# Performance work log

Hardware: AMD Instinct MI355X
Metric: run time of the kernel (lower is better)

## Reference

```python
import jax, jax.numpy as jnp
import numpy as np

NLAT = 192  # octahedral O96-class grid


def _lons(nlat):
    half = [20 + 4 * i for i in range(nlat // 2)]
    return half + half[::-1]


def _dft_matrix(nlat, mmax):
    # Truncated per-ring real-DFT basis (torch.fft.rfft convention, 'forward' 1/n norm).
    # Ring j has nlon_j points; frequencies beyond its Nyquist (m > nlon_j//2) are zero.
    lons = _lons(nlat)
    max_nlon = max(lons)
    D = np.zeros((nlat, max_nlon, mmax), dtype=np.complex64)
    for j, n in enumerate(lons):
        keep = min(mmax, n // 2 + 1)
        k = np.arange(n)[:, None]
        m = np.arange(keep)[None, :]
        D[j, :n, :keep] = np.exp(-2j * np.pi * k * m / n) / n
    return D


def _legendre_weights(nlat, lmax, mmax):
    # Orthonormalized associated Legendre P_l^m at Gaussian latitudes (north->south),
    # with Gaussian quadrature weights and the 2*pi longitude factor folded in.
    xg, wg = np.polynomial.legendre.leggauss(nlat)
    x = xg[::-1].copy()
    w = wg[::-1].copy()
    s = np.sqrt(1.0 - x * x)
    leg = np.zeros((lmax, mmax, nlat))
    pmm = np.full(nlat, 1.0 / np.sqrt(4.0 * np.pi))
    for m in range(mmax):
        if m > 0:
            pmm = -np.sqrt((2 * m + 1) / (2.0 * m)) * s * pmm
        if m < lmax:
            leg[m, m] = pmm
        if m + 1 < lmax:
            leg[m + 1, m] = np.sqrt(2 * m + 3.0) * x * pmm
        for l in range(m + 2, lmax):
            a = np.sqrt((4.0 * l * l - 1.0) / (l * l - m * m))
            bb = np.sqrt(((2.0 * l + 1.0) * (l - 1 + m) * (l - 1 - m)) / ((2.0 * l - 3.0) * (l * l - m * m)))
            leg[l, m] = a * x * leg[l - 1, m] - bb * leg[l - 2, m]
    leg = 2.0 * np.pi * leg * w[None, None, :]
    return leg.astype(np.float32)


def setup_inputs() -> dict:
    key = jax.random.key(0)
    nlat = NLAT
    lmax = mmax = nlat // 2
    n_points = sum(_lons(nlat))  # 40320 for nlat=192
    data = jax.random.normal(key, (4, 1, 1, n_points, 100), dtype=jnp.float32)
    dft = jnp.asarray(_dft_matrix(nlat, mmax))
    leg = jnp.asarray(_legendre_weights(nlat, lmax, mmax))
    return {"data": data, "dft": dft, "leg": leg}


def reference(data, dft, leg):
    b, t, e, p, v = data.shape
    nlat, max_nlon, mmax = dft.shape
    lmax = leg.shape[0]
    lons = _lons(nlat)
    # static scatter map: flattened ragged rings -> [nlat, max_nlon] padded layout
    flat_idx = np.concatenate([j * max_nlon + np.arange(n) for j, n in enumerate(lons)])
    x = jnp.transpose(data, (0, 1, 2, 4, 3)).reshape(-1, p)  # [(b t e v), p]
    B = x.shape[0]
    x_pad = jnp.zeros((B, nlat * max_nlon), x.dtype).at[:, flat_idx].set(x)
    x_pad = x_pad.reshape(B, nlat, max_nlon)
    # ragged per-ring truncated real DFT, then associated-Legendre contraction
    f_hat = jnp.einsum('bjn,jnm->bjm', x_pad, dft)        # [B, nlat, mmax] complex
    coeffs = jnp.einsum('bjm,lmj->blm', f_hat, leg)       # [B, lmax, mmax] complex
    coeffs = coeffs.reshape(b, t, e, v, lmax, mmax)
    return jnp.transpose(coeffs, (0, 1, 2, 4, 5, 3))      # [b, t, e, yF, xF, v]
```

## Files before the change

### kernel.cpp

```cpp
#include <hip/hip_runtime.h>

#define NLAT 192
#define NPTS 40320
#define MMAX 96
#define LMAX 96
#define NV   100
#define MAXN 400
#define NB   400

typedef __attribute__((ext_vector_type(8))) short short8v;
typedef __attribute__((ext_vector_type(4))) float f32x4;

#define FSTR 40

static __device__ __forceinline__ float bits2f(unsigned int b) {
    union { unsigned int i; float f; } v; v.i = b; return v.f;
}
static __device__ __forceinline__ unsigned int f2bf(float f) {
    union { float f; unsigned int i; } v; v.f = f;
    return (v.i + 0x7FFFu + ((v.i >> 16) & 1u)) >> 16;
}

static __device__ __forceinline__ int Ssum(int n) {
    int q = n >> 3, r = n & 7; return 4 * q * (q - 1) + q * r;
}
static __device__ __forceinline__ int atoffk(int j) {
    if (j < 96) return 32 * (Ssum(j + 12) - 4);
    return 32 * (672 + 676 - Ssum(204 - j));
}
static __device__ __forceinline__ int kpad_of(int j) {
    return 32 * ((j < 96 ? (j + 12) : (203 - j)) >> 3);
}

typedef const __attribute__((address_space(1))) void* gas_ptr;
typedef __attribute__((address_space(3))) void* las_ptr;
static __device__ __forceinline__ void gload_lds16(const void* g, void* l) {
    __builtin_amdgcn_global_load_lds((gas_ptr)g, (las_ptr)l, 16, 0, 0);
}

__global__ __launch_bounds__(256) void leg_conv_kernel(
    const float* __restrict__ leg,
    unsigned short* __restrict__ legh,
    unsigned short* __restrict__ legl)
{
    int idx = blockIdx.x * 256 + threadIdx.x;
    if (idx >= 96 * 96 * 192) return;
    int j = idx % 192;
    int lm = idx / 192;
    int m = lm % 96, l = lm / 96;
    float v = leg[idx];
    unsigned int h = f2bf(v);
    unsigned int lo = f2bf(v - bits2f(h << 16));
    size_t o = ((size_t)m * 96 + l) * 192 + j;
    legh[o] = (unsigned short)h;
    legl[o] = (unsigned short)lo;
}

__global__ __launch_bounds__(256) void dft_transpose_kernel(
    const unsigned int* __restrict__ dftw,
    unsigned short* __restrict__ At)
{
    const int j = blockIdx.x;
    const int kpad = kpad_of(j);
    const int t = blockIdx.y;
    const int k0 = t * 32;
    if (k0 >= kpad) return;
    const int n = j < 96 ? 20 + 4 * j : 400 - 4 * (j - 96);
    unsigned short* abase = At + (size_t)atoffk(j) * 192 + (size_t)t * 6144;
    const int tid = threadIdx.x;
#pragma unroll
    for (int s = 0; s < 3; ++s) {
        int slot = s * 256 + tid;
        int row = slot % 192;
        int ch  = slot / 192;
        int m = row < 96 ? row : row - 96;
        bool isIm = row >= 96;
        const unsigned int* dp = dftw + ((size_t)j * MAXN + k0 + ch * 8) * 96 + m;
        unsigned short o[8];
#pragma unroll
        for (int i = 0; i < 8; ++i) {
            int k = k0 + ch * 8 + i;
            unsigned int v = (k < n) ? dp[(size_t)i * 96] : 0u;
            o[i] = isIm ? (unsigned short)(v >> 16) : (unsigned short)(v & 0xFFFFu);
        }
        uint4 pk;
        pk.x = (unsigned int)o[0] | ((unsigned int)o[1] << 16);
        pk.y = (unsigned int)o[2] | ((unsigned int)o[3] << 16);
        pk.z = (unsigned int)o[4] | ((unsigned int)o[5] << 16);
        pk.w = (unsigned int)o[6] | ((unsigned int)o[7] << 16);
        *(uint4*)(abase + (size_t)row * 32 + ch * 8) = pk;
    }
}

__global__ __launch_bounds__(256, 4) void dft_mfma_kernel(
    const float* __restrict__ data,
    const unsigned short* __restrict__ At,
    unsigned short* __restrict__ fh_hi,
    unsigned short* __restrict__ fh_lo,
    int c0, int cn)
{
    __shared__ unsigned short A_lds[2][192 * 32];
    __shared__ unsigned short Xh_lds[2][64 * 32];
    __shared__ unsigned short Xl_lds[2][64 * 32];

    const int id  = blockIdx.x;
    const int j   = id % 192;
    const int bt  = id / 192;
    const int tid = threadIdx.x;
    const int w   = tid >> 6;
    const int l   = tid & 63;
    const int lr  = l & 15;
    const int kg  = l >> 4;
    const int kgp = kg ^ ((lr >> 1) & 3);

    int n, start;
    if (j < 96) { n = 20 + 4 * j; start = 2 * j * j + 18 * j; }
    else { int jj = j - 96; n = 400 - 4 * jj; start = 20160 + 402 * jj - 2 * jj * jj; }
    const int nsteps = kpad_of(j) >> 5;
    const unsigned short* abase = At + (size_t)atoffk(j) * 192;

    const int Bb = c0 + bt * 50;
    const int bb = Bb / NV;
    const int vb = Bb % NV;
    const float* dbase = data + (size_t)bb * NPTS * NV + vb;

    const int xc  = tid >> 2;
    const int xch = tid & 3;
    const int xpc = xch ^ ((xc >> 1) & 3);

    f32x4 acc[3][4];
#pragma unroll
    for (int i = 0; i < 3; ++i)
#pragma unroll
        for (int nt = 0; nt < 4; ++nt) acc[i][nt] = (f32x4){0.f, 0.f, 0.f, 0.f};

    float xv[8];

    {
        const float* sp = dbase + (size_t)(start + xch * 8) * NV + xc;
#pragma unroll
        for (int i = 0; i < 8; ++i) {
            int k = xch * 8 + i;
            xv[i] = (xc < 50 && k < n) ? sp[(size_t)i * NV] : 0.f;
        }
#pragma unroll
        for (int s = 0; s < 3; ++s) {
            int slot = s * 256 + tid;
            int row  = slot >> 2;
            int chs  = (slot & 3) ^ ((row >> 1) & 3);
            gload_lds16(abase + (size_t)row * 32 + chs * 8, &A_lds[0][s * 2048 + w * 512]);
        }
        unsigned int hi4[4], lo4[4];
#pragma unroll
        for (int t2 = 0; t2 < 4; ++t2) {
            unsigned int x0 = __float_as_uint(xv[2 * t2]);
            unsigned int x1 = __float_as_uint(xv[2 * t2 + 1]);
            hi4[t2] = __builtin_amdgcn_perm(x1, x0, 0x07060302u);
            float r0 = xv[2 * t2]     - bits2f(x0 & 0xFFFF0000u);
            float r1 = xv[2 * t2 + 1] - bits2f(x1 & 0xFFFF0000u);
            unsigned int pk;
            asm("v_cvt_pk_bf16_f32 %0, %1, %2" : "=v"(pk) : "v"(r0), "v"(r1));
            lo4[t2] = pk;
        }
        *(uint4*)&Xh_lds[0][xc * 32 + xpc * 8] = (uint4){hi4[0], hi4[1], hi4[2], hi4[3]};
        *(uint4*)&Xl_lds[0][xc * 32 + xpc * 8] = (uint4){lo4[0], lo4[1], lo4[2], lo4[3]};
        __syncthreads();
    }

    int buf = 0;
    for (int t = 0; t < nsteps; ++t) {
        const int nb = buf ^ 1;
        const bool pf = (t + 1 < nsteps);

        if (pf) {
            const float* sp = dbase + (size_t)(start + (t + 1) * 32 + xch * 8) * NV + xc;
#pragma unroll
            for (int i = 0; i < 8; ++i) {
                int k = (t + 1) * 32 + xch * 8 + i;
                xv[i] = (xc < 50 && k < n) ? sp[(size_t)i * NV] : 0.f;
            }
#pragma unroll
            for (int s = 0; s < 3; ++s) {
                int slot = s * 256 + tid;
                int row  = slot >> 2;
                int chs  = (slot & 3) ^ ((row >> 1) & 3);
                gload_lds16(abase + (size_t)(t + 1) * 6144 + row * 32 + chs * 8,
                            &A_lds[nb][s * 2048 + w * 512]);
            }
        }

        short8v a0 = *(const short8v*)&A_lds[buf][((3 * w + 0) * 16 + lr) * 32 + kgp * 8];
        short8v a1 = *(const short8v*)&A_lds[buf][((3 * w + 1) * 16 + lr) * 32 + kgp * 8];
        short8v a2 = *(const short8v*)&A_lds[buf][((3 * w + 2) * 16 + lr) * 32 + kgp * 8];
#pragma unroll
        for (int nt = 0; nt < 4; ++nt) {
            short8v bh = *(const short8v*)&Xh_lds[buf][(nt * 16 + lr) * 32 + kgp * 8];
            short8v bl = *(const short8v*)&Xl_lds[buf][(nt * 16 + lr) * 32 + kgp * 8];
            acc[0][nt] = __builtin_amdgcn_mfma_f32_16x16x32_bf16(a0, bh, acc[0][nt], 0, 0, 0);
            acc[1][nt] = __builtin_amdgcn_mfma_f32_16x16x32_bf16(a1, bh, acc[1][nt], 0, 0, 0);
            acc[2][nt] = __builtin_amdgcn_mfma_f32_16x16x32_bf16(a2, bh, acc[2][nt], 0, 0, 0);
            acc[0][nt] = __builtin_amdgcn_mfma_f32_16x16x32_bf16(a0, bl, acc[0][nt], 0, 0, 0);
            acc[1][nt] = __builtin_amdgcn_mfma_f32_16x16x32_bf16(a1, bl, acc[1][nt], 0, 0, 0);
            acc[2][nt] = __builtin_amdgcn_mfma_f32_16x16x32_bf16(a2, bl, acc[2][nt], 0, 0, 0);
        }

        if (pf) {
            unsigned int hi4[4], lo4[4];
#pragma unroll
            for (int t2 = 0; t2 < 4; ++t2) {
                unsigned int x0 = __float_as_uint(xv[2 * t2]);
                unsigned int x1 = __float_as_uint(xv[2 * t2 + 1]);
                hi4[t2] = __builtin_amdgcn_perm(x1, x0, 0x07060302u);
                float r0 = xv[2 * t2]     - bits2f(x0 & 0xFFFF0000u);
                float r1 = xv[2 * t2 + 1] - bits2f(x1 & 0xFFFF0000u);
                unsigned int pk;
                asm("v_cvt_pk_bf16_f32 %0, %1, %2" : "=v"(pk) : "v"(r0), "v"(r1));
                lo4[t2] = pk;
            }
            *(uint4*)&Xh_lds[nb][xc * 32 + xpc * 8] = (uint4){hi4[0], hi4[1], hi4[2], hi4[3]};
            *(uint4*)&Xl_lds[nb][xc * 32 + xpc * 8] = (uint4){lo4[0], lo4[1], lo4[2], lo4[3]};
        }
        __syncthreads();
        buf = nb;
    }

#pragma unroll
    for (int i = 0; i < 3; ++i)
#pragma unroll
        for (int nt = 0; nt < 4; ++nt) {
            int c = nt * 16 + lr;
            if (c < 50) {
                int Brel = bt * 50 + c;
                int mm0 = (3 * w + i) * 16 + kg * 4;
                unsigned short* oh = fh_hi + ((size_t)j * 192 + mm0) * cn + Brel;
                unsigned short* ol = fh_lo + ((size_t)j * 192 + mm0) * cn + Brel;
#pragma unroll
                for (int r = 0; r < 4; ++r) {
                    float v = acc[i][nt][r];
                    unsigned int h = f2bf(v);
                    unsigned int lo = f2bf(v - bits2f(h << 16));
                    oh[(size_t)r * cn] = (unsigned short)h;
                    ol[(size_t)r * cn] = (unsigned short)lo;
                }
            }
        }
}

__global__ __launch_bounds__(256) void leg_mfma_kernel(
    const unsigned short* __restrict__ legh,
    const unsigned short* __restrict__ legl,
    const unsigned short* __restrict__ fh_hi,
    const unsigned short* __restrict__ fh_lo,
    unsigned int* __restrict__ out,
    int c0, int cn)
{
    __shared__ unsigned short A_lds[2 * 96 * FSTR];
    __shared__ unsigned short F_lds[2 * 2 * 64 * FSTR];

    const int m   = blockIdx.x;
    const int bt  = blockIdx.y;
    const int tid = threadIdx.x;
    const int w   = tid >> 6;
    const int l   = tid & 63;
    const int lr  = l & 15;
    const int kg  = l >> 4;

    f32x4 acc[6][2];
#pragma unroll
    for (int lt = 0; lt < 6; ++lt)
#pragma unroll
        for (int pl = 0; pl < 2; ++pl) acc[lt][pl] = (f32x4){0.f, 0.f, 0.f, 0.f};

    const unsigned int* lh32 = (const unsigned int*)legh;
    const unsigned int* ll32 = (const unsigned int*)legl;

    for (int j0 = 0; j0 < NLAT; j0 += 32) {
        __syncthreads();

#pragma unroll
        for (int s = 0; s < 12; ++s) {
            const int hl = (s >= 6) ? 1 : 0;
            int rem = tid + 256 * s - 1536 * hl;
            int lrow = rem >> 4;
            int ku = rem & 15;
            const unsigned int* src = hl ? ll32 : lh32;
            unsigned int v = src[((size_t)m * 96 + lrow) * 96 + (j0 >> 1) + ku];
            ((unsigned int*)A_lds)[(size_t)hl * 96 * (FSTR / 2) + lrow * (FSTR / 2) + ku] = v;
        }

#pragma unroll
        for (int s = 0; s < 13; ++s) {
            int q = tid + 256 * s;
            if (q < 3200) {
                int u  = q % 25;
                int r2 = q / 25;
                int jj = r2 & 31;
                int r3 = r2 >> 5;
                int pl = r3 & 1;
                int hl = r3 >> 1;
                const unsigned short* src = hl ? fh_lo : fh_hi;
                const unsigned int* s32 = (const unsigned int*)src;
                unsigned int v = s32[((size_t)(j0 + jj) * 192 + m + 96 * pl) * (cn >> 1)
                                     + bt * 25 + u];
                size_t base = ((size_t)(pl * 2 + hl) * 64 + 2 * u) * FSTR + jj;
                F_lds[base]        = (unsigned short)(v & 0xFFFFu);
                F_lds[base + FSTR] = (unsigned short)(v >> 16);
            }
        }
        __syncthreads();

        short8v fH[2], fL[2];
#pragma unroll
        for (int pl = 0; pl < 2; ++pl) {
            fH[pl] = *(const short8v*)&F_lds[((size_t)(pl * 2 + 0) * 64 + w * 16 + lr) * FSTR + kg * 8];
            fL[pl] = *(const short8v*)&F_lds[((size_t)(pl * 2 + 1) * 64 + w * 16 + lr) * FSTR + kg * 8];
        }
#pragma unroll
        for (int lt = 0; lt < 6; ++lt) {
            short8v ah = *(const short8v*)&A_lds[(size_t)(0 * 96 + lt * 16 + lr) * FSTR + kg * 8];
            short8v al = *(const short8v*)&A_lds[(size_t)(1 * 96 + lt * 16 + lr) * FSTR + kg * 8];
#pragma unroll
            for (int pl = 0; pl < 2; ++pl) {
                acc[lt][pl] = __builtin_amdgcn_mfma_f32_16x16x32_bf16(ah, fH[pl], acc[lt][pl], 0, 0, 0);
                acc[lt][pl] = __builtin_amdgcn_mfma_f32_16x16x32_bf16(ah, fL[pl], acc[lt][pl], 0, 0, 0);
                acc[lt][pl] = __builtin_amdgcn_mfma_f32_16x16x32_bf16(al, fH[pl], acc[lt][pl], 0, 0, 0);
            }
        }
    }

    int c = w * 16 + lr;
    if (c < 50) {
        int B = c0 + bt * 50 + c;
        int bb = B / NV, vv = B % NV;
#pragma unroll
        for (int lt = 0; lt < 6; ++lt) {
#pragma unroll
            for (int r = 0; r < 4; ++r) {
                int ll = lt * 16 + kg * 4 + r;
                out[(((size_t)bb * LMAX + ll) * MMAX + m) * NV + vv] =
                    f2bf(acc[lt][0][r]) | (f2bf(acc[lt][1][r]) << 16);
            }
        }
    }
}

extern "C" void kernel_launch(void* const* d_in, const int* in_sizes, int n_in,
                              void* d_out, int out_size, void* d_ws, size_t ws_size,
                              hipStream_t stream) {
    if (n_in != 3) return;

    const float* data = (const float*)d_in[0];
    const unsigned int* dftw = (const unsigned int*)d_in[1];
    const float* leg  = (const float*)d_in[2];
    unsigned int* out = (unsigned int*)d_out;

    const size_t LEGN = (size_t)96 * 96 * 192;
    const size_t LEGB = 2 * LEGN * sizeof(unsigned short);
    const size_t ATN  = (size_t)43008 * 192;
    const size_t ATB  = ATN * sizeof(unsigned short);
    const size_t rowb = (size_t)192 * 192 * 2 * sizeof(unsigned short);
    if (ws_size < LEGB + ATB + 50 * rowb) return;

    unsigned short* legh = (unsigned short*)d_ws;
    unsigned short* legl = legh + LEGN;
    unsigned short* At   = legl + LEGN;

    size_t maxrows = (ws_size - LEGB - ATB) / rowb;
    int chunk = (int)((maxrows / 50) * 50);
    if (chunk > NB) chunk = NB;

    leg_conv_kernel<<<dim3((96 * 96 * 192 + 255) / 256), dim3(256), 0, stream>>>(
        leg, legh, legl);
    dft_transpose_kernel<<<dim3(192, 13), dim3(256), 0, stream>>>(dftw, At);

    for (int c0 = 0; c0 < NB; c0 += chunk) {
        int cn = NB - c0 < chunk ? NB - c0 : chunk;
        unsigned short* fh_hi = At + ATN;
        unsigned short* fh_lo = fh_hi + (size_t)192 * 192 * cn;

        int nbt = cn / 50;
        dim3 g1(192 * nbt);
        dft_mfma_kernel<<<g1, dim3(256), 0, stream>>>(data, At, fh_hi, fh_lo, c0, cn);
        dim3 g2(96, nbt);
        leg_mfma_kernel<<<g2, dim3(256), 0, stream>>>(legh, legl, fh_hi, fh_lo, out, c0, cn);
    }
}
```

Baseline: 87.08 us.

## Switch DFT and Legendre MFMA paths from split bf16 to fp16

```diff
diff --git a/kernel.cpp b/kernel.cpp
--- a/kernel.cpp
+++ b/kernel.cpp
@@ -8,7 +8,7 @@
 #define MAXN 400
 #define NB   400
 
-typedef __attribute__((ext_vector_type(8))) short short8v;
+typedef __attribute__((ext_vector_type(8))) _Float16 half8v;
 typedef __attribute__((ext_vector_type(4))) float f32x4;
 
 #define FSTR 40
@@ -20,6 +20,13 @@
     union { float f; unsigned int i; } v; v.f = f;
     return (v.i + 0x7FFFu + ((v.i >> 16) & 1u)) >> 16;
 }
+static __device__ __forceinline__ unsigned short f2h(float f) {
+    _Float16 h = (_Float16)f;
+    union { _Float16 h; unsigned short s; } u; u.h = h; return u.s;
+}
+static __device__ __forceinline__ float h2f(unsigned short s) {
+    union { _Float16 h; unsigned short s; } u; u.s = s; return (float)u.h;
+}
 
 static __device__ __forceinline__ int Ssum(int n) {
     int q = n >> 3, r = n & 7; return 4 * q * (q - 1) + q * r;
@@ -30,12 +37,6 @@
 }
 static __device__ __forceinline__ int kpad_of(int j) {
     return 32 * ((j < 96 ? (j + 12) : (203 - j)) >> 3);
-}
-
-typedef const __attribute__((address_space(1))) void* gas_ptr;
-typedef __attribute__((address_space(3))) void* las_ptr;
-static __device__ __forceinline__ void gload_lds16(const void* g, void* l) {
-    __builtin_amdgcn_global_load_lds((gas_ptr)g, (las_ptr)l, 16, 0, 0);
 }
 
 __global__ __launch_bounds__(256) void leg_conv_kernel(
@@ -49,11 +50,11 @@
     int lm = idx / 192;
     int m = lm % 96, l = lm / 96;
     float v = leg[idx];
-    unsigned int h = f2bf(v);
-    unsigned int lo = f2bf(v - bits2f(h << 16));
+    unsigned short h = f2h(v);
+    unsigned short lo = f2h(v - h2f(h));
     size_t o = ((size_t)m * 96 + l) * 192 + j;
-    legh[o] = (unsigned short)h;
-    legl[o] = (unsigned short)lo;
+    legh[o] = h;
+    legl[o] = lo;
 }
 
 __global__ __launch_bounds__(256) void dft_transpose_kernel(
@@ -81,7 +82,8 @@
         for (int i = 0; i < 8; ++i) {
             int k = k0 + ch * 8 + i;
             unsigned int v = (k < n) ? dp[(size_t)i * 96] : 0u;
-            o[i] = isIm ? (unsigned short)(v >> 16) : (unsigned short)(v & 0xFFFFu);
+            float f = isIm ? bits2f(v & 0xFFFF0000u) : bits2f(v << 16);
+            o[i] = f2h(f);
         }
         uint4 pk;
         pk.x = (unsigned int)o[0] | ((unsigned int)o[1] << 16);
@@ -92,14 +94,12 @@
     }
 }
 
-__global__ __launch_bounds__(256, 4) void dft_mfma_kernel(
+__global__ __launch_bounds__(256) void dft_mfma_kernel(
     const float* __restrict__ data,
     const unsigned short* __restrict__ At,
-    unsigned short* __restrict__ fh_hi,
-    unsigned short* __restrict__ fh_lo,
+    unsigned short* __restrict__ fh,
     int c0, int cn)
 {
-    __shared__ unsigned short A_lds[2][192 * 32];
     __shared__ unsigned short Xh_lds[2][64 * 32];
     __shared__ unsigned short Xl_lds[2][64 * 32];
 
@@ -143,27 +143,17 @@
             int k = xch * 8 + i;
             xv[i] = (xc < 50 && k < n) ? sp[(size_t)i * NV] : 0.f;
         }
-#pragma unroll
-        for (int s = 0; s < 3; ++s) {
-            int slot = s * 256 + tid;
-            int row  = slot >> 2;
-            int chs  = (slot & 3) ^ ((row >> 1) & 3);
-            gload_lds16(abase + (size_t)row * 32 + chs * 8, &A_lds[0][s * 2048 + w * 512]);
-        }
-        unsigned int hi4[4], lo4[4];
+        unsigned int hw[4], lw[4];
 #pragma unroll
         for (int t2 = 0; t2 < 4; ++t2) {
-            unsigned int x0 = __float_as_uint(xv[2 * t2]);
-            unsigned int x1 = __float_as_uint(xv[2 * t2 + 1]);
-            hi4[t2] = __builtin_amdgcn_perm(x1, x0, 0x07060302u);
-            float r0 = xv[2 * t2]     - bits2f(x0 & 0xFFFF0000u);
-            float r1 = xv[2 * t2 + 1] - bits2f(x1 & 0xFFFF0000u);
-            unsigned int pk;
-            asm("v_cvt_pk_bf16_f32 %0, %1, %2" : "=v"(pk) : "v"(r0), "v"(r1));
-            lo4[t2] = pk;
-        }
-        *(uint4*)&Xh_lds[0][xc * 32 + xpc * 8] = (uint4){hi4[0], hi4[1], hi4[2], hi4[3]};
-        *(uint4*)&Xl_lds[0][xc * 32 + xpc * 8] = (uint4){lo4[0], lo4[1], lo4[2], lo4[3]};
+            unsigned short h0 = f2h(xv[2 * t2]), h1 = f2h(xv[2 * t2 + 1]);
+            unsigned short l0 = f2h(xv[2 * t2] - h2f(h0));
+            unsigned short l1 = f2h(xv[2 * t2 + 1] - h2f(h1));
+            hw[t2] = (unsigned int)h0 | ((unsigned int)h1 << 16);
+            lw[t2] = (unsigned int)l0 | ((unsigned int)l1 << 16);
+        }
+        *(uint4*)&Xh_lds[0][xc * 32 + xpc * 8] = (uint4){hw[0], hw[1], hw[2], hw[3]};
+        *(uint4*)&Xl_lds[0][xc * 32 + xpc * 8] = (uint4){lw[0], lw[1], lw[2], lw[3]};
         __syncthreads();
     }
 
@@ -179,46 +169,37 @@
                 int k = (t + 1) * 32 + xch * 8 + i;
                 xv[i] = (xc < 50 && k < n) ? sp[(size_t)i * NV] : 0.f;
             }
-#pragma unroll
-            for (int s = 0; s < 3; ++s) {
-                int slot = s * 256 + tid;
-                int row  = slot >> 2;
-                int chs  = (slot & 3) ^ ((row >> 1) & 3);
-                gload_lds16(abase + (size_t)(t + 1) * 6144 + row * 32 + chs * 8,
-                            &A_lds[nb][s * 2048 + w * 512]);
-            }
-        }
-
-        short8v a0 = *(const short8v*)&A_lds[buf][((3 * w + 0) * 16 + lr) * 32 + kgp * 8];
-        short8v a1 = *(const short8v*)&A_lds[buf][((3 * w + 1) * 16 + lr) * 32 + kgp * 8];
-        short8v a2 = *(const short8v*)&A_lds[buf][((3 * w + 2) * 16 + lr) * 32 + kgp * 8];
+        }
+
+        const half8v* av = (const half8v*)(abase + (size_t)t * 6144);
+        half8v a0 = av[((3 * w + 0) * 16 + lr) * 4 + kg];
+        half8v a1 = av[((3 * w + 1) * 16 + lr) * 4 + kg];
+        half8v a2 = av[((3 * w + 2) * 16 + lr) * 4 + kg];
+
 #pragma unroll
         for (int nt = 0; nt < 4; ++nt) {
-            short8v bh = *(const short8v*)&Xh_lds[buf][(nt * 16 + lr) * 32 + kgp * 8];
-            short8v bl = *(const short8v*)&Xl_lds[buf][(nt * 16 + lr) * 32 + kgp * 8];
-            acc[0][nt] = __builtin_amdgcn_mfma_f32_16x16x32_bf16(a0, bh, acc[0][nt], 0, 0, 0);
-            acc[1][nt] = __builtin_amdgcn_mfma_f32_16x16x32_bf16(a1, bh, acc[1][nt], 0, 0, 0);
-            acc[2][nt] = __builtin_amdgcn_mfma_f32_16x16x32_bf16(a2, bh, acc[2][nt], 0, 0, 0);
-            acc[0][nt] = __builtin_amdgcn_mfma_f32_16x16x32_bf16(a0, bl, acc[0][nt], 0, 0, 0);
-            acc[1][nt] = __builtin_amdgcn_mfma_f32_16x16x32_bf16(a1, bl, acc[1][nt], 0, 0, 0);
-            acc[2][nt] = __builtin_amdgcn_mfma_f32_16x16x32_bf16(a2, bl, acc[2][nt], 0, 0, 0);
+            half8v bh = *(const half8v*)&Xh_lds[buf][(nt * 16 + lr) * 32 + kgp * 8];
+            half8v bl = *(const half8v*)&Xl_lds[buf][(nt * 16 + lr) * 32 + kgp * 8];
+            acc[0][nt] = __builtin_amdgcn_mfma_f32_16x16x32_f16(a0, bh, acc[0][nt], 0, 0, 0);
+            acc[1][nt] = __builtin_amdgcn_mfma_f32_16x16x32_f16(a1, bh, acc[1][nt], 0, 0, 0);
+            acc[2][nt] = __builtin_amdgcn_mfma_f32_16x16x32_f16(a2, bh, acc[2][nt], 0, 0, 0);
+            acc[0][nt] = __builtin_amdgcn_mfma_f32_16x16x32_f16(a0, bl, acc[0][nt], 0, 0, 0);
+            acc[1][nt] = __builtin_amdgcn_mfma_f32_16x16x32_f16(a1, bl, acc[1][nt], 0, 0, 0);
+            acc[2][nt] = __builtin_amdgcn_mfma_f32_16x16x32_f16(a2, bl, acc[2][nt], 0, 0, 0);
         }
 
         if (pf) {
-            unsigned int hi4[4], lo4[4];
+            unsigned int hw[4], lw[4];
 #pragma unroll
             for (int t2 = 0; t2 < 4; ++t2) {
-                unsigned int x0 = __float_as_uint(xv[2 * t2]);
-                unsigned int x1 = __float_as_uint(xv[2 * t2 + 1]);
-                hi4[t2] = __builtin_amdgcn_perm(x1, x0, 0x07060302u);
-                float r0 = xv[2 * t2]     - bits2f(x0 & 0xFFFF0000u);
-                float r1 = xv[2 * t2 + 1] - bits2f(x1 & 0xFFFF0000u);
-                unsigned int pk;
-                asm("v_cvt_pk_bf16_f32 %0, %1, %2" : "=v"(pk) : "v"(r0), "v"(r1));
-                lo4[t2] = pk;
-            }
-            *(uint4*)&Xh_lds[nb][xc * 32 + xpc * 8] = (uint4){hi4[0], hi4[1], hi4[2], hi4[3]};
-            *(uint4*)&Xl_lds[nb][xc * 32 + xpc * 8] = (uint4){lo4[0], lo4[1], lo4[2], lo4[3]};
+                unsigned short h0 = f2h(xv[2 * t2]), h1 = f2h(xv[2 * t2 + 1]);
+                unsigned short l0 = f2h(xv[2 * t2] - h2f(h0));
+                unsigned short l1 = f2h(xv[2 * t2 + 1] - h2f(h1));
+                hw[t2] = (unsigned int)h0 | ((unsigned int)h1 << 16);
+                lw[t2] = (unsigned int)l0 | ((unsigned int)l1 << 16);
+            }
+            *(uint4*)&Xh_lds[nb][xc * 32 + xpc * 8] = (uint4){hw[0], hw[1], hw[2], hw[3]};
+            *(uint4*)&Xl_lds[nb][xc * 32 + xpc * 8] = (uint4){lw[0], lw[1], lw[2], lw[3]};
         }
         __syncthreads();
         buf = nb;
@@ -232,16 +213,10 @@
             if (c < 50) {
                 int Brel = bt * 50 + c;
                 int mm0 = (3 * w + i) * 16 + kg * 4;
-                unsigned short* oh = fh_hi + ((size_t)j * 192 + mm0) * cn + Brel;
-                unsigned short* ol = fh_lo + ((size_t)j * 192 + mm0) * cn + Brel;
-#pragma unroll
-                for (int r = 0; r < 4; ++r) {
-                    float v = acc[i][nt][r];
-                    unsigned int h = f2bf(v);
-                    unsigned int lo = f2bf(v - bits2f(h << 16));
-                    oh[(size_t)r * cn] = (unsigned short)h;
-                    ol[(size_t)r * cn] = (unsigned short)lo;
-                }
+                unsigned short* oh = fh + ((size_t)j * 192 + mm0) * cn + Brel;
+#pragma unroll
+                for (int r = 0; r < 4; ++r)
+                    oh[(size_t)r * cn] = f2h(acc[i][nt][r]);
             }
         }
 }
@@ -249,13 +224,12 @@
 __global__ __launch_bounds__(256) void leg_mfma_kernel(
     const unsigned short* __restrict__ legh,
     const unsigned short* __restrict__ legl,
-    const unsigned short* __restrict__ fh_hi,
-    const unsigned short* __restrict__ fh_lo,
+    const unsigned short* __restrict__ fh,
     unsigned int* __restrict__ out,
     int c0, int cn)
 {
     __shared__ unsigned short A_lds[2 * 96 * FSTR];
-    __shared__ unsigned short F_lds[2 * 2 * 64 * FSTR];
+    __shared__ unsigned short F_lds[2 * 64 * FSTR];
 
     const int m   = blockIdx.x;
     const int bt  = blockIdx.y;
@@ -273,6 +247,7 @@
 
     const unsigned int* lh32 = (const unsigned int*)legh;
     const unsigned int* ll32 = (const unsigned int*)legl;
+    const unsigned int* f32p = (const unsigned int*)fh;
 
     for (int j0 = 0; j0 < NLAT; j0 += 32) {
         __syncthreads();
@@ -289,41 +264,34 @@
         }
 
 #pragma unroll
-        for (int s = 0; s < 13; ++s) {
+        for (int s = 0; s < 7; ++s) {
             int q = tid + 256 * s;
-            if (q < 3200) {
+            if (q < 1600) {
                 int u  = q % 25;
                 int r2 = q / 25;
                 int jj = r2 & 31;
-                int r3 = r2 >> 5;
-                int pl = r3 & 1;
-                int hl = r3 >> 1;
-                const unsigned short* src = hl ? fh_lo : fh_hi;
-                const unsigned int* s32 = (const unsigned int*)src;
-                unsigned int v = s32[((size_t)(j0 + jj) * 192 + m + 96 * pl) * (cn >> 1)
-                                     + bt * 25 + u];
-                size_t base = ((size_t)(pl * 2 + hl) * 64 + 2 * u) * FSTR + jj;
+                int pl = r2 >> 5;
+                unsigned int v = f32p[((size_t)(j0 + jj) * 192 + m + 96 * pl) * (cn >> 1)
+                                      + bt * 25 + u];
+                size_t base = ((size_t)pl * 64 + 2 * u) * FSTR + jj;
                 F_lds[base]        = (unsigned short)(v & 0xFFFFu);
                 F_lds[base + FSTR] = (unsigned short)(v >> 16);
             }
         }
         __syncthreads();
 
-        short8v fH[2], fL[2];
-#pragma unroll
-        for (int pl = 0; pl < 2; ++pl) {
-            fH[pl] = *(const short8v*)&F_lds[((size_t)(pl * 2 + 0) * 64 + w * 16 + lr) * FSTR + kg * 8];
-            fL[pl] = *(const short8v*)&F_lds[((size_t)(pl * 2 + 1) * 64 + w * 16 + lr) * FSTR + kg * 8];
-        }
+        half8v fF[2];
+#pragma unroll
+        for (int pl = 0; pl < 2; ++pl)
+            fF[pl] = *(const half8v*)&F_lds[((size_t)pl * 64 + w * 16 + lr) * FSTR + kg * 8];
 #pragma unroll
         for (int lt = 0; lt < 6; ++lt) {
-            short8v ah = *(const short8v*)&A_lds[(size_t)(0 * 96 + lt * 16 + lr) * FSTR + kg * 8];
-            short8v al = *(const short8v*)&A_lds[(size_t)(1 * 96 + lt * 16 + lr) * FSTR + kg * 8];
+            half8v ah = *(const half8v*)&A_lds[(size_t)(0 * 96 + lt * 16 + lr) * FSTR + kg * 8];
+            half8v al = *(const half8v*)&A_lds[(size_t)(1 * 96 + lt * 16 + lr) * FSTR + kg * 8];
 #pragma unroll
             for (int pl = 0; pl < 2; ++pl) {
-                acc[lt][pl] = __builtin_amdgcn_mfma_f32_16x16x32_bf16(ah, fH[pl], acc[lt][pl], 0, 0, 0);
-                acc[lt][pl] = __builtin_amdgcn_mfma_f32_16x16x32_bf16(ah, fL[pl], acc[lt][pl], 0, 0, 0);
-                acc[lt][pl] = __builtin_amdgcn_mfma_f32_16x16x32_bf16(al, fH[pl], acc[lt][pl], 0, 0, 0);
+                acc[lt][pl] = __builtin_amdgcn_mfma_f32_16x16x32_f16(ah, fF[pl], acc[lt][pl], 0, 0, 0);
+                acc[lt][pl] = __builtin_amdgcn_mfma_f32_16x16x32_f16(al, fF[pl], acc[lt][pl], 0, 0, 0);
             }
         }
     }
@@ -358,7 +326,7 @@
     const size_t LEGB = 2 * LEGN * sizeof(unsigned short);
     const size_t ATN  = (size_t)43008 * 192;
     const size_t ATB  = ATN * sizeof(unsigned short);
-    const size_t rowb = (size_t)192 * 192 * 2 * sizeof(unsigned short);
+    const size_t rowb = (size_t)192 * 192 * sizeof(unsigned short);
     if (ws_size < LEGB + ATB + 50 * rowb) return;
 
     unsigned short* legh = (unsigned short*)d_ws;
@@ -375,13 +343,12 @@
 
     for (int c0 = 0; c0 < NB; c0 += chunk) {
         int cn = NB - c0 < chunk ? NB - c0 : chunk;
-        unsigned short* fh_hi = At + ATN;
-        unsigned short* fh_lo = fh_hi + (size_t)192 * 192 * cn;
+        unsigned short* fh = At + ATN;
 
         int nbt = cn / 50;
         dim3 g1(192 * nbt);
-        dft_mfma_kernel<<<g1, dim3(256), 0, stream>>>(data, At, fh_hi, fh_lo, c0, cn);
+        dft_mfma_kernel<<<g1, dim3(256), 0, stream>>>(data, At, fh, c0, cn);
         dim3 g2(96, nbt);
-        leg_mfma_kernel<<<g2, dim3(256), 0, stream>>>(legh, legl, fh_hi, fh_lo, out, c0, cn);
-    }
-}
+        leg_mfma_kernel<<<g2, dim3(256), 0, stream>>>(legh, legl, fh, out, c0, cn);
+    }
+}
```

Measured after the change: 90.93 us. 4.4% more time.
